# Kernel tuning notes

Measured on AMD Instinct MI355X. Metric: run time of the kernel, lower is better.

Reference implementation:

```python
import jax, jax.numpy as jnp
import numpy as np

B, N, D, T, M, V, K, HB, FF, L, H = 64, 32, 512, 8, 20, 512, 8, 16, 2048, 2, 8
SCALE = 1.0 / np.sqrt(D // H)


def _ln(x, g, b, eps=1e-5):
    m = x.mean(-1, keepdims=True)
    v = ((x - m) ** 2).mean(-1, keepdims=True)
    return (x - m) / jnp.sqrt(v + eps) * g + b


def _heads(x):
    return x.reshape(x.shape[:-1] + (H, D // H))


def setup_inputs():
    ks = iter(jax.random.split(jax.random.key(0), 60))
    def rn(shape, s=1.0):
        return jax.random.normal(next(ks), shape, jnp.float32) * s
    d = {}
    d['ego_query'] = rn((B, 1, D))
    d['agents_query'] = rn((B, N, D))
    d['bev_feature'] = rn((B, D, HB, HB))
    d['agent_states'] = rn((B, N, 8)) * 10.0
    d['agent_labels'] = rn((B, N))
    d['gt_traj'] = rn((B, T, 3))
    d['codebook'] = rn((V, 2), 0.1)
    for p in ['ego_ctx', 'bevproj', 'agent']:
        d[p + '_w'] = rn((D, D), 0.02); d[p + '_b'] = jnp.zeros((D,))
        d[p + '_g'] = jnp.ones((D,)); d[p + '_beta'] = jnp.zeros((D,))
    d['tok_emb'] = rn((V, D), 0.02)
    d['step_e'] = rn((T, D), 0.02)
    d['mode_e'] = rn((M, D), 0.02)
    d['role_e'] = rn((2, D), 0.02)
    d['bos_e'] = rn((1, D), 0.02)
    for p in ['t', 'e', 'v']:
        d[p + '_qkv_w'] = rn((L, 3 * D, D), 0.02); d[p + '_qkv_b'] = jnp.zeros((L, 3 * D))
        d[p + '_out_w'] = rn((L, D, D), 0.02); d[p + '_out_b'] = jnp.zeros((L, D))
        d[p + '_g'] = jnp.ones((L, D)); d[p + '_beta'] = jnp.zeros((L, D))
    d['ffn_w1'] = rn((L, FF, D), 0.02); d['ffn_b1'] = jnp.zeros((L, FF))
    d['ffn_w2'] = rn((L, D, FF), 0.02); d['ffn_b2'] = jnp.zeros((L, D))
    d['ffn_g'] = jnp.ones((L, D)); d['ffn_beta'] = jnp.zeros((L, D))
    d['head_w'] = rn((V, D), 0.02); d['head_b'] = jnp.zeros((V,))
    return d


def reference(ego_query, agents_query, bev_feature, agent_states, agent_labels, gt_traj, codebook,
              ego_ctx_w, ego_ctx_b, ego_ctx_g, ego_ctx_beta,
              bevproj_w, bevproj_b, bevproj_g, bevproj_beta,
              agent_w, agent_b, agent_g, agent_beta,
              tok_emb, step_e, mode_e, role_e, bos_e,
              t_qkv_w, t_qkv_b, t_out_w, t_out_b, t_g, t_beta,
              e_qkv_w, e_qkv_b, e_out_w, e_out_b, e_g, e_beta,
              v_qkv_w, v_qkv_b, v_out_w, v_out_b, v_g, v_beta,
              ffn_w1, ffn_b1, ffn_w2, ffn_b2, ffn_g, ffn_beta,
              head_w, head_b):
    Bd = ego_query.shape[0]
    P = HB * HB
    # BEV tokens [B, P, D]
    bev = jnp.transpose(bev_feature.reshape(Bd, D, P), (0, 2, 1))
    bev = jax.nn.relu(_ln(bev @ bevproj_w.T + bevproj_b, bevproj_g, bevproj_beta))
    # top-K nearest valid agents
    valid = jax.nn.sigmoid(agent_labels) > 0.05
    dist = jnp.where(valid, jnp.linalg.norm(agent_states[..., :2], axis=-1), jnp.inf)
    _, idx = jax.lax.top_k(-dist, K)
    topk_valid = jnp.take_along_axis(valid, idx, axis=1)
    agent_ctx = jnp.take_along_axis(agents_query, idx[..., None], axis=1)  # [B,K,D]
    agent_enc = jax.nn.relu(_ln(agent_ctx @ agent_w.T + agent_b, agent_g, agent_beta))
    agent_kv = agent_enc[:, :, None, :] + step_e[None, None] + role_e[1][None, None, None]  # [B,K,T,D]
    ego_base = jax.nn.relu(_ln(ego_query[:, 0] @ ego_ctx_w.T + ego_ctx_b, ego_ctx_g, ego_ctx_beta))
    # sequential codebook matching (accumulated-position NN scan, no grad)
    gt_pos = jnp.broadcast_to(gt_traj[:, None, :, :2], (Bd, M, T, 2))
    cb = jax.lax.stop_gradient(codebook)
    def cb_step(acc, pos_t):
        dsq = ((acc[:, :, None, :] + cb[None, None] - pos_t[:, :, None, :]) ** 2).sum(-1)  # [B,M,V]
        ii = jnp.argmin(dsq, axis=-1)
        return acc + cb[ii], ii
    _, idxs = jax.lax.scan(cb_step, jnp.zeros((Bd, M, 2), gt_pos.dtype),
                           jnp.moveaxis(jax.lax.stop_gradient(gt_pos), 2, 0))
    tokens = jnp.transpose(idxs, (1, 2, 0))  # [B,M,T]
    # teacher-forced input embeddings
    bos = bos_e[0][None, :] + ego_base  # [B,D]
    inp = jnp.concatenate([jnp.broadcast_to(bos[:, None, None, :], (Bd, M, 1, D)),
                           tok_emb[tokens[:, :, :-1]]], axis=2)
    ego_q = inp + step_e[None, None] + role_e[0][None, None, None] + mode_e[None, :, None, :]
    caus = jnp.triu(jnp.full((T, T), -jnp.inf, ego_q.dtype), 1)
    inv = ~topk_valid
    inv = inv & ~inv.all(axis=-1, keepdims=True)  # guard: never mask everything
    for i in range(L):
        # temporal causal self-attention over T
        qw, kw, vw = jnp.split(t_qkv_w[i], 3, 0); qb, kb, vb = jnp.split(t_qkv_b[i], 3, 0)
        Q, Kh, Vh = _heads(ego_q @ qw.T + qb), _heads(ego_q @ kw.T + kb), _heads(ego_q @ vw.T + vb)
        s = jnp.einsum('bmqhe,bmkhe->bmhqk', Q, Kh) * SCALE + caus
        o = jnp.einsum('bmhqk,bmkhe->bmqhe', jax.nn.softmax(s, -1), Vh).reshape(ego_q.shape)
        ego_q = _ln(ego_q + o @ t_out_w[i].T + t_out_b[i], t_g[i], t_beta[i])
        # ego-to-agent cross-attention (kv varies per step t)
        qw, kw, vw = jnp.split(e_qkv_w[i], 3, 0); qb, kb, vb = jnp.split(e_qkv_b[i], 3, 0)
        Q = _heads(ego_q @ qw.T + qb)  # [B,M,T,H,e]
        Kh, Vh = _heads(agent_kv @ kw.T + kb), _heads(agent_kv @ vw.T + vb)  # [B,K,T,H,e]
        s = jnp.einsum('bmthe,bkthe->bmhtk', Q, Kh) * SCALE
        s = jnp.where(inv[:, None, None, None, :], -jnp.inf, s)
        o = jnp.einsum('bmhtk,bkthe->bmthe', jax.nn.softmax(s, -1), Vh).reshape(ego_q.shape)
        ego_q = _ln(ego_q + o @ e_out_w[i].T + e_out_b[i], e_g[i], e_beta[i])
        # BEV cross-attention
        qw, kw, vw = jnp.split(v_qkv_w[i], 3, 0); qb, kb, vb = jnp.split(v_qkv_b[i], 3, 0)
        Q = _heads(ego_q @ qw.T + qb)
        Kh, Vh = _heads(bev @ kw.T + kb), _heads(bev @ vw.T + vb)  # [B,P,H,e]
        s = jnp.einsum('bmthe,bphe->bmhtp', Q, Kh) * SCALE
        o = jnp.einsum('bmhtp,bphe->bmthe', jax.nn.softmax(s, -1), Vh).reshape(ego_q.shape)
        ego_q = _ln(ego_q + o @ v_out_w[i].T + v_out_b[i], v_g[i], v_beta[i])
        # FFN
        hid = jax.nn.gelu(ego_q @ ffn_w1[i].T + ffn_b1[i], approximate=False)
        ego_q = _ln(ego_q + hid @ ffn_w2[i].T + ffn_b2[i], ffn_g[i], ffn_beta[i])
    return ego_q @ head_w.T + head_b  # token logits [B,M,T,V]
```

## Files before the change

kernel.cpp:

```cpp
#include <hip/hip_runtime.h>
#include <hip/hip_bf16.h>
#include <math.h>
#include <type_traits>

typedef __hip_bfloat16 bf16;
typedef __attribute__((ext_vector_type(8))) short bf16x8;
typedef __attribute__((ext_vector_type(4))) float f32x4;

__device__ __forceinline__ float b2f(bf16 x){ return __bfloat162float(x); }
__device__ __forceinline__ short f2s(float f){
  bf16 h = __float2bfloat16(f);
  short s; __builtin_memcpy(&s, &h, 2); return s;
}
__device__ __forceinline__ float u2f(unsigned short u){ union { unsigned int i; float f; } z; z.i = ((unsigned int)u) << 16; return z.f; }
__device__ __forceinline__ bf16x8 cvt8(float4 a, float4 b){
  return (bf16x8){f2s(a.x),f2s(a.y),f2s(a.z),f2s(a.w), f2s(b.x),f2s(b.y),f2s(b.z),f2s(b.w)};
}

struct WSrc { const float* p[12]; };
__global__ __launch_bounds__(256) void k_cvtw(WSrc srcs, bf16* __restrict__ dst){
  const unsigned off[13] = {0u,262144u,524288u,786432u,2359296u,2883584u,4456448u,4980736u,
                            6553600u,7077888u,9175040u,11272192u,11534336u};
  size_t base = ((size_t)blockIdx.x*256 + threadIdx.x)*8;
  int seg = 0;
  while (seg < 11 && base >= off[seg+1]) seg++;
  const float* s = srcs.p[seg] + (base - off[seg]);
  float4 a = *(const float4*)s;
  float4 b = *(const float4*)(s + 4);
  *(bf16x8*)&dst[base] = cvt8(a, b);
}

template<typename AT, typename WT, typename CT, int ACT, int BN, int RES>
__global__ __launch_bounds__(256, BN == 64 ? 2 : 1)
void k_gemm_mfma(const AT* __restrict__ A, const WT* __restrict__ W,
                 const float* __restrict__ bias, CT* C,
                 const float* Rres, int rows, int Kd, int Nc)
{
  __shared__ short As[128][40];
  __shared__ short Bs[BN][40];
  constexpr int NI = BN / 32;
  int rb = blockIdx.x * 128, nb = blockIdx.y * BN;
  int tid = threadIdx.x;
  int l = tid & 63, w = tid >> 6;
  int wr = (w >> 1) * 64, wc = (w & 1) * (BN/2);
  int lr = l & 15, lk = l >> 4;
  f32x4 acc[4][NI];
  #pragma unroll
  for (int i = 0; i < 4; i++)
    #pragma unroll
    for (int j = 0; j < NI; j++)
      acc[i][j] = (f32x4){0.f, 0.f, 0.f, 0.f};
  int sr = tid >> 1;
  int sc = (tid & 1) * 16;
  bool doB = (BN == 128) || (tid < 128);
  bool doA = (rb + sr) < rows;

  float4 faA[4], fbA[4], faB[4], fbB[4];
  bf16x8 baA[2], baB[2], wbA[2], wbB[2];
  #pragma unroll
  for (int i = 0; i < 4; i++){ faA[i] = (float4){0,0,0,0}; fbA[i] = (float4){0,0,0,0};
                               faB[i] = (float4){0,0,0,0}; fbB[i] = (float4){0,0,0,0}; }
  baA[0] = baA[1] = baB[0] = baB[1] = (bf16x8){0,0,0,0,0,0,0,0};
  wbA[0] = wbA[1] = wbB[0] = wbB[1] = (bf16x8){0,0,0,0,0,0,0,0};

  auto LOADS = [&](float4* fa, bf16x8* ba, float4* fb, bf16x8* wb, int k0){
    if constexpr (std::is_same<AT, float>::value){
      if (doA){
        const float4* p = (const float4*)(A + (size_t)(rb + sr)*Kd + k0 + sc);
        fa[0] = p[0]; fa[1] = p[1]; fa[2] = p[2]; fa[3] = p[3];
      }
    } else {
      if (doA){
        const bf16x8* p = (const bf16x8*)((const unsigned short*)A + (size_t)(rb + sr)*Kd + k0 + sc);
        ba[0] = p[0]; ba[1] = p[1];
      }
    }
    if (doB){
      if constexpr (std::is_same<WT, float>::value){
        const float4* p = (const float4*)(W + (size_t)(nb + sr)*Kd + k0 + sc);
        fb[0] = p[0]; fb[1] = p[1]; fb[2] = p[2]; fb[3] = p[3];
      } else {
        const bf16x8* p = (const bf16x8*)((const unsigned short*)W + (size_t)(nb + sr)*Kd + k0 + sc);
        wb[0] = p[0]; wb[1] = p[1];
      }
    }
  };
  auto STOREK = [&](float4* fa, bf16x8* ba, float4* fb, bf16x8* wb){
    if constexpr (std::is_same<AT, float>::value){
      *(bf16x8*)&As[sr][sc]     = cvt8(fa[0], fa[1]);
      *(bf16x8*)&As[sr][sc + 8] = cvt8(fa[2], fa[3]);
    } else {
      *(bf16x8*)&As[sr][sc]     = ba[0];
      *(bf16x8*)&As[sr][sc + 8] = ba[1];
    }
    if (doB){
      if constexpr (std::is_same<WT, float>::value){
        *(bf16x8*)&Bs[sr][sc]     = cvt8(fb[0], fb[1]);
        *(bf16x8*)&Bs[sr][sc + 8] = cvt8(fb[2], fb[3]);
      } else {
        *(bf16x8*)&Bs[sr][sc]     = wb[0];
        *(bf16x8*)&Bs[sr][sc + 8] = wb[1];
      }
    }
  };
  auto COMPUTE = [&](){
    bf16x8 af[4], bf_[NI];
    #pragma unroll
    for (int mi = 0; mi < 4; mi++) af[mi]  = *(const bf16x8*)&As[wr + mi*16 + lr][lk*8];
    #pragma unroll
    for (int ni = 0; ni < NI; ni++) bf_[ni] = *(const bf16x8*)&Bs[wc + ni*16 + lr][lk*8];
    #pragma unroll
    for (int mi = 0; mi < 4; mi++)
      #pragma unroll
      for (int ni = 0; ni < NI; ni++)
        acc[mi][ni] = __builtin_amdgcn_mfma_f32_16x16x32_bf16(af[mi], bf_[ni], acc[mi][ni], 0, 0, 0);
  };

  int nst = Kd >> 5;
  LOADS(faA, baA, fbA, wbA, 0);
  LOADS(faB, baB, fbB, wbB, 32);
  for (int s = 0; s < nst; s += 2){
    __syncthreads();
    STOREK(faA, baA, fbA, wbA);
    __syncthreads();
    if (s + 2 < nst) LOADS(faA, baA, fbA, wbA, (s+2)*32);
    COMPUTE();
    __syncthreads();
    STOREK(faB, baB, fbB, wbB);
    __syncthreads();
    if (s + 3 < nst) LOADS(faB, baB, fbB, wbB, (s+3)*32);
    COMPUTE();
  }

  #pragma unroll
  for (int mi = 0; mi < 4; mi++){
    #pragma unroll
    for (int ni = 0; ni < NI; ni++){
      int col = nb + wc + ni*16 + lr;
      float bs = bias[col];
      #pragma unroll
      for (int r = 0; r < 4; r++){
        int row = rb + wr + mi*16 + lk*4 + r;
        if (row < rows){
          float v = acc[mi][ni][r] + bs;
          if (RES) v += Rres[(size_t)row*Nc + col];
          if (ACT == 1) v = 0.5f*v*(1.0f + erff(v*0.70710678118654752f));
          if constexpr (std::is_same<CT, float>::value) C[(size_t)row*Nc + col] = v;
          else C[(size_t)row*Nc + col] = __float2bfloat16(v);
        }
      }
    }
  }
}

template<typename AT, typename WT, typename CT, int ACT, int RES>
__global__ __launch_bounds__(256, 4)
void k_gemm64(const AT* __restrict__ A, const WT* __restrict__ W,
              const float* __restrict__ bias, CT* C,
              const float* Rres, int rows, int Kd, int Nc)
{
  __shared__ short As[64][40];
  __shared__ short Bs[64][40];
  int rb = blockIdx.x * 64, nb = blockIdx.y * 64;
  int tid = threadIdx.x;
  int l = tid & 63, w = tid >> 6;
  int wr = (w >> 1) * 32, wc = (w & 1) * 32;
  int lr = l & 15, lk = l >> 4;
  f32x4 acc[2][2];
  #pragma unroll
  for (int i = 0; i < 2; i++)
    #pragma unroll
    for (int j = 0; j < 2; j++)
      acc[i][j] = (f32x4){0.f, 0.f, 0.f, 0.f};
  int sr = tid >> 2;
  int sc = (tid & 3) * 8;
  bool doA = (rb + sr) < rows;

  float4 faA[2], faB[2], fwA[2], fwB[2];
  bf16x8 baA, baB, wbA, wbB;
  faA[0]=faA[1]=faB[0]=faB[1]=(float4){0,0,0,0};
  fwA[0]=fwA[1]=fwB[0]=fwB[1]=(float4){0,0,0,0};
  baA = baB = wbA = wbB = (bf16x8){0,0,0,0,0,0,0,0};

  auto LOADS = [&](float4* fa, bf16x8& ba, float4* fw, bf16x8& wb, int k0){
    if constexpr (std::is_same<AT, float>::value){
      if (doA){
        const float4* p = (const float4*)(A + (size_t)(rb + sr)*Kd + k0 + sc);
        fa[0] = p[0]; fa[1] = p[1];
      }
    } else {
      if (doA) ba = *(const bf16x8*)((const unsigned short*)A + (size_t)(rb + sr)*Kd + k0 + sc);
    }
    if constexpr (std::is_same<WT, float>::value){
      const float4* p = (const float4*)(W + (size_t)(nb + sr)*Kd + k0 + sc);
      fw[0] = p[0]; fw[1] = p[1];
    } else {
      wb = *(const bf16x8*)((const unsigned short*)W + (size_t)(nb + sr)*Kd + k0 + sc);
    }
  };
  auto STOREK = [&](float4* fa, bf16x8& ba, float4* fw, bf16x8& wb){
    if constexpr (std::is_same<AT, float>::value) *(bf16x8*)&As[sr][sc] = cvt8(fa[0], fa[1]);
    else                                          *(bf16x8*)&As[sr][sc] = ba;
    if constexpr (std::is_same<WT, float>::value) *(bf16x8*)&Bs[sr][sc] = cvt8(fw[0], fw[1]);
    else                                          *(bf16x8*)&Bs[sr][sc] = wb;
  };
  auto COMPUTE = [&](){
    bf16x8 af[2], bf_[2];
    #pragma unroll
    for (int mi = 0; mi < 2; mi++) af[mi]  = *(const bf16x8*)&As[wr + mi*16 + lr][lk*8];
    #pragma unroll
    for (int ni = 0; ni < 2; ni++) bf_[ni] = *(const bf16x8*)&Bs[wc + ni*16 + lr][lk*8];
    #pragma unroll
    for (int mi = 0; mi < 2; mi++)
      #pragma unroll
      for (int ni = 0; ni < 2; ni++)
        acc[mi][ni] = __builtin_amdgcn_mfma_f32_16x16x32_bf16(af[mi], bf_[ni], acc[mi][ni], 0, 0, 0);
  };

  int nst = Kd >> 5;
  LOADS(faA, baA, fwA, wbA, 0);
  LOADS(faB, baB, fwB, wbB, 32);
  for (int s = 0; s < nst; s += 2){
    __syncthreads();
    STOREK(faA, baA, fwA, wbA);
    __syncthreads();
    if (s + 2 < nst) LOADS(faA, baA, fwA, wbA, (s+2)*32);
    COMPUTE();
    __syncthreads();
    STOREK(faB, baB, fwB, wbB);
    __syncthreads();
    if (s + 3 < nst) LOADS(faB, baB, fwB, wbB, (s+3)*32);
    COMPUTE();
  }

  #pragma unroll
  for (int mi = 0; mi < 2; mi++){
    #pragma unroll
    for (int ni = 0; ni < 2; ni++){
      int col = nb + wc + ni*16 + lr;
      float bs = bias[col];
      #pragma unroll
      for (int r = 0; r < 4; r++){
        int row = rb + wr + mi*16 + lk*4 + r;
        if (row < rows){
          float v = acc[mi][ni][r] + bs;
          if (RES) v += Rres[(size_t)row*Nc + col];
          if (ACT == 1) v = 0.5f*v*(1.0f + erff(v*0.70710678118654752f));
          if constexpr (std::is_same<CT, float>::value) C[(size_t)row*Nc + col] = v;
          else C[(size_t)row*Nc + col] = __float2bfloat16(v);
        }
      }
    }
  }
}

template<typename XT, typename OT>
__global__ __launch_bounds__(256) void k_ln(const XT* X, const float* R,
                                            const float* g, const float* bt,
                                            OT* out, int relu)
{
  __shared__ float red[4];
  int row = blockIdx.x, t = threadIdx.x;
  size_t base = (size_t)row * 512;
  float x0, x1;
  if constexpr (std::is_same<XT, float>::value){ x0 = X[base + t]; x1 = X[base + t + 256]; }
  else { x0 = b2f(X[base + t]); x1 = b2f(X[base + t + 256]); }
  if (R){ x0 += R[base + t]; x1 += R[base + t + 256]; }
  float v = x0 + x1;
  #pragma unroll
  for (int o = 32; o > 0; o >>= 1) v += __shfl_xor(v, o);
  if ((t & 63) == 0) red[t >> 6] = v;
  __syncthreads();
  float mean = (red[0]+red[1]+red[2]+red[3]) * (1.0f/512.0f);
  float d0 = x0 - mean, d1 = x1 - mean;
  v = d0*d0 + d1*d1;
  #pragma unroll
  for (int o = 32; o > 0; o >>= 1) v += __shfl_xor(v, o);
  __syncthreads();
  if ((t & 63) == 0) red[t >> 6] = v;
  __syncthreads();
  float var = (red[0]+red[1]+red[2]+red[3]) * (1.0f/512.0f);
  float is = 1.0f / sqrtf(var + 1e-5f);
  float y0 = d0*is*g[t] + bt[t];
  float y1 = d1*is*g[t+256] + bt[t+256];
  if (relu){ y0 = fmaxf(y0, 0.0f); y1 = fmaxf(y1, 0.0f); }
  if constexpr (std::is_same<OT, float>::value){ out[base + t] = y0; out[base + t + 256] = y1; }
  else { out[base + t] = __float2bfloat16(y0); out[base + t + 256] = __float2bfloat16(y1); }
}

__global__ void k_bev_tok(const float* __restrict__ bev, bf16* __restrict__ out){
  __shared__ float tile[32][33];
  int b = blockIdx.z;
  int d0 = blockIdx.x * 32;
  int p0 = blockIdx.y * 32;
  int tx = threadIdx.x, ty = threadIdx.y;
  #pragma unroll
  for (int i = 0; i < 4; i++){
    int d = d0 + ty + i*8;
    tile[ty + i*8][tx] = bev[((size_t)b*512 + d)*256 + p0 + tx];
  }
  __syncthreads();
  #pragma unroll
  for (int i = 0; i < 4; i++){
    int p = p0 + ty + i*8;
    out[((size_t)b*256 + p)*512 + d0 + tx] = __float2bfloat16(tile[tx][ty + i*8]);
  }
}

__global__ void k_topk(const float* __restrict__ labels, const float* __restrict__ states,
                       int* __restrict__ idxo, int* __restrict__ invo)
{
  __shared__ float dist[32];
  __shared__ int valid[32];
  int b = blockIdx.x, t = threadIdx.x;
  if (t < 32){
    float lab = labels[b*32 + t];
    float sg = 1.0f / (1.0f + expf(-lab));
    int va = sg > 0.05f;
    float x = states[((size_t)b*32 + t)*8 + 0];
    float y = states[((size_t)b*32 + t)*8 + 1];
    float d = sqrtf(__fadd_rn(__fmul_rn(x,x), __fmul_rn(y,y)));
    dist[t] = va ? d : INFINITY;
    valid[t] = va;
  }
  __syncthreads();
  if (t == 0){
    unsigned used = 0;
    int inv8[8]; int allinv = 1;
    for (int kk = 0; kk < 8; kk++){
      float best = INFINITY; int bi = -1;
      for (int i = 0; i < 32; i++){
        if (used & (1u << i)) continue;
        if (bi < 0 || dist[i] < best){ best = dist[i]; bi = i; }
      }
      used |= 1u << bi;
      idxo[b*8 + kk] = bi;
      inv8[kk] = !valid[bi];
      allinv &= inv8[kk];
    }
    for (int kk = 0; kk < 8; kk++) invo[b*8 + kk] = allinv ? 0 : inv8[kk];
  }
}

__global__ void k_gather(const float* __restrict__ aq, const int* __restrict__ idx, bf16* __restrict__ out)
{
  int rk = blockIdx.x; int b = rk >> 3;
  int src = idx[rk] & 31;
  int t = threadIdx.x;
  size_t sbase = ((size_t)(b*32 + src))*512;
  out[(size_t)rk*512 + t]       = __float2bfloat16(aq[sbase + t]);
  out[(size_t)rk*512 + t + 256] = __float2bfloat16(aq[sbase + t + 256]);
}

__global__ void k_agentkv(const float* __restrict__ enc, const float* __restrict__ step_e,
                          const float* __restrict__ role_e, bf16* __restrict__ out)
{
  int row = blockIdx.x;
  int t8 = row & 7; int bk = row >> 3;
  int tx = threadIdx.x;
  #pragma unroll
  for (int j = 0; j < 2; j++){
    int d = tx + j*256;
    out[(size_t)row*512 + d] = __float2bfloat16((enc[(size_t)bk*512 + d] + step_e[t8*512 + d]) + role_e[512 + d]);
  }
}

__global__ __launch_bounds__(64) void k_cbscan(const float* __restrict__ gt, const float* __restrict__ cb,
                                               int* __restrict__ toks)
{
  __shared__ float cbx[512], cby[512];
  int b = blockIdx.x;
  int l = threadIdx.x;
  #pragma unroll
  for (int i = 0; i < 8; i++){
    int v = l + i*64;
    cbx[v] = cb[v*2 + 0];
    cby[v] = cb[v*2 + 1];
  }
  __syncthreads();
  float ax = 0.0f, ay = 0.0f;
  for (int t = 0; t < 8; t++){
    float px = gt[(b*8 + t)*3 + 0];
    float py = gt[(b*8 + t)*3 + 1];
    float bestv = INFINITY; int besti = 0;
    #pragma unroll
    for (int i = 0; i < 8; i++){
      int v = l*8 + i;
      float dx = __fsub_rn(__fadd_rn(ax, cbx[v]), px);
      float dy = __fsub_rn(__fadd_rn(ay, cby[v]), py);
      float d = __fadd_rn(__fmul_rn(dx,dx), __fmul_rn(dy,dy));
      if (d < bestv || (d == bestv && v < besti)){ bestv = d; besti = v; }
    }
    #pragma unroll
    for (int o = 32; o > 0; o >>= 1){
      float ov = __shfl_xor(bestv, o);
      int oi = __shfl_xor(besti, o);
      if (ov < bestv || (ov == bestv && oi < besti)){ bestv = ov; besti = oi; }
    }
    ax = __fadd_rn(ax, cbx[besti]);
    ay = __fadd_rn(ay, cby[besti]);
    if (l == 0) toks[b*8 + t] = besti;
  }
}

__global__ void k_embed(const int* __restrict__ toks, const float* __restrict__ ebase,
                        const float* __restrict__ tok_emb, const float* __restrict__ step_e,
                        const float* __restrict__ mode_e, const float* __restrict__ role_e,
                        const float* __restrict__ bos_e, float* __restrict__ out)
{
  int row = blockIdx.x;
  int t = row & 7; int bm = row >> 3; int m = bm % 20; int b = bm / 20;
  int tok = (t == 0) ? 0 : (toks[b*8 + t - 1] & 511);
  int tx = threadIdx.x;
  #pragma unroll
  for (int j = 0; j < 2; j++){
    int d = tx + j*256;
    float base = (t == 0) ? (bos_e[d] + ebase[(size_t)b*512 + d])
                          : tok_emb[(size_t)tok*512 + d];
    out[(size_t)row*512 + d] = ((base + step_e[t*512 + d]) + role_e[d]) + mode_e[m*512 + d];
  }
}

__global__ __launch_bounds__(64) void k_tattn(const bf16* __restrict__ QKV, bf16* __restrict__ O)
{
  __shared__ float q[8][65], k[8][65], v[8][65], w[8][9];
  int h = blockIdx.x & 7; int bm = blockIdx.x >> 3;
  int l = threadIdx.x;
  for (int t = 0; t < 8; t++){
    size_t base = ((size_t)(bm*8 + t))*1536 + h*64 + l;
    q[t][l] = b2f(QKV[base]);
    k[t][l] = b2f(QKV[base + 512]);
    v[t][l] = b2f(QKV[base + 1024]);
  }
  __syncthreads();
  int tq = l >> 3, tk = l & 7;
  float s = -INFINITY;
  if (tk <= tq){
    float acc = 0.0f;
    #pragma unroll
    for (int e = 0; e < 64; e++) acc += q[tq][e]*k[tk][e];
    s = acc * 0.125f;
  }
  float mx = s;
  #pragma unroll
  for (int o = 1; o < 8; o <<= 1) mx = fmaxf(mx, __shfl_xor(mx, o));
  float ex = (tk <= tq) ? expf(s - mx) : 0.0f;
  float sm = ex;
  #pragma unroll
  for (int o = 1; o < 8; o <<= 1) sm += __shfl_xor(sm, o);
  w[tq][tk] = ex / sm;
  __syncthreads();
  #pragma unroll
  for (int t2 = 0; t2 < 8; t2++){
    float acc = 0.0f;
    #pragma unroll
    for (int tk2 = 0; tk2 < 8; tk2++) acc += w[t2][tk2]*v[tk2][l];
    O[((size_t)(bm*8 + t2))*512 + h*64 + l] = __float2bfloat16(acc);
  }
}

__global__ __launch_bounds__(64) void k_eattn(const bf16* __restrict__ Q, const bf16* __restrict__ KV,
                                              const int* __restrict__ inv,
                                              bf16* __restrict__ O, int row0)
{
  int blk = blockIdx.x;
  int h = blockIdx.y;
  int grow = row0 + blk;
  int t = grow & 7;
  int b = grow / 160;
  int l = threadIdx.x;
  size_t qoff = (size_t)blk*512 + h*64 + l;
  float q = b2f(Q[qoff]);
  float s[8];
  #pragma unroll
  for (int k = 0; k < 8; k++){
    float p = q * b2f(KV[((size_t)((b*8 + k)*8 + t))*1024 + h*64 + l]);
    #pragma unroll
    for (int o = 32; o > 0; o >>= 1) p += __shfl_xor(p, o);
    s[k] = p * 0.125f;
  }
  float mx = -INFINITY;
  #pragma unroll
  for (int k = 0; k < 8; k++){
    if (inv[b*8 + k]) s[k] = -INFINITY;
    mx = fmaxf(mx, s[k]);
  }
  float sum = 0.0f, w[8];
  #pragma unroll
  for (int k = 0; k < 8; k++){ w[k] = expf(s[k] - mx); sum += w[k]; }
  float rs = 1.0f / sum;
  float acc = 0.0f;
  #pragma unroll
  for (int k = 0; k < 8; k++)
    acc += (w[k]*rs) * b2f(KV[((size_t)((b*8 + k)*8 + t))*1024 + 512 + h*64 + l]);
  O[qoff] = __float2bfloat16(acc);
}

__global__ __launch_bounds__(256, 2) void k_vattn(const bf16* __restrict__ Q, const bf16* __restrict__ KV,
                                                  bf16* __restrict__ O)
{
  __shared__ unsigned short Ks[256][72];
  __shared__ unsigned short Vt[64][264];
  __shared__ float red[2][2][16];
  unsigned short (*P_lds)[264] = (unsigned short (*)[264])&Ks[0][0];

  int bl = blockIdx.x, h = blockIdx.y, qz = blockIdx.z;
  int tid = threadIdx.x;
  const unsigned short* KVr = (const unsigned short*)KV;

  {
    const uint4* ksrc = (const uint4*)&KVr[((size_t)(bl*256 + tid))*1024 + h*64];
    const uint4* vsrc = (const uint4*)&KVr[((size_t)(bl*256 + tid))*1024 + 512 + h*64];
    #pragma unroll
    for (int i = 0; i < 8; i++){
      uint4 kx = ksrc[i];
      *(uint4*)&Ks[tid][i*8] = kx;
    }
    #pragma unroll
    for (int i = 0; i < 8; i++){
      uint4 vx = vsrc[i];
      unsigned short vs[8];
      __builtin_memcpy(vs, &vx, 16);
      #pragma unroll
      for (int j = 0; j < 8; j++) Vt[i*8 + j][tid] = vs[j];
    }
  }
  __syncthreads();

  int w = tid >> 6, l = tid & 63, lr = l & 15, lk = l >> 4;
  int mt = w >> 1, ch = w & 1;

  int qrow = bl*160 + qz*32 + mt*16 + lr;
  const unsigned short* Qr = (const unsigned short*)Q;
  bf16x8 qf0 = *(const bf16x8*)&Qr[(size_t)qrow*512 + h*64 + lk*8];
  bf16x8 qf1 = *(const bf16x8*)&Qr[(size_t)qrow*512 + h*64 + 32 + lk*8];

  f32x4 sacc[8];
  #pragma unroll
  for (int nt = 0; nt < 8; nt++) sacc[nt] = (f32x4){0.f,0.f,0.f,0.f};
  #pragma unroll
  for (int nt = 0; nt < 8; nt++){
    int key0 = ch*128 + nt*16 + lr;
    bf16x8 kf0 = *(const bf16x8*)&Ks[key0][lk*8];
    bf16x8 kf1 = *(const bf16x8*)&Ks[key0][32 + lk*8];
    sacc[nt] = __builtin_amdgcn_mfma_f32_16x16x32_bf16(qf0, kf0, sacc[nt], 0, 0, 0);
    sacc[nt] = __builtin_amdgcn_mfma_f32_16x16x32_bf16(qf1, kf1, sacc[nt], 0, 0, 0);
  }

  float rmax[4] = {-INFINITY, -INFINITY, -INFINITY, -INFINITY};
  #pragma unroll
  for (int nt = 0; nt < 8; nt++)
    #pragma unroll
    for (int r = 0; r < 4; r++){
      float v = sacc[nt][r] * 0.125f;
      sacc[nt][r] = v;
      rmax[r] = fmaxf(rmax[r], v);
    }
  #pragma unroll
  for (int r = 0; r < 4; r++){
    #pragma unroll
    for (int o = 1; o < 16; o <<= 1) rmax[r] = fmaxf(rmax[r], __shfl_xor(rmax[r], o));
  }
  if (lr == 0){
    #pragma unroll
    for (int r = 0; r < 4; r++) red[mt][ch][lk*4 + r] = rmax[r];
  }
  __syncthreads();
  float m4[4];
  #pragma unroll
  for (int r = 0; r < 4; r++) m4[r] = fmaxf(red[mt][0][lk*4 + r], red[mt][1][lk*4 + r]);
  float rsum[4] = {0.f, 0.f, 0.f, 0.f};
  #pragma unroll
  for (int nt = 0; nt < 8; nt++){
    #pragma unroll
    for (int r = 0; r < 4; r++){
      float e = expf(sacc[nt][r] - m4[r]);
      rsum[r] += e;
      P_lds[mt*16 + lk*4 + r][ch*128 + nt*16 + lr] = (unsigned short)f2s(e);
    }
  }
  #pragma unroll
  for (int r = 0; r < 4; r++){
    #pragma unroll
    for (int o = 1; o < 16; o <<= 1) rsum[r] += __shfl_xor(rsum[r], o);
  }
  __syncthreads();
  if (lr == 0){
    #pragma unroll
    for (int r = 0; r < 4; r++) red[mt][ch][lk*4 + r] = rsum[r];
  }
  __syncthreads();
  float rcp4[4];
  #pragma unroll
  for (int r = 0; r < 4; r++) rcp4[r] = 1.0f / (red[mt][0][lk*4 + r] + red[mt][1][lk*4 + r]);

  f32x4 oacc0 = (f32x4){0.f,0.f,0.f,0.f};
  f32x4 oacc1 = (f32x4){0.f,0.f,0.f,0.f};
  #pragma unroll
  for (int kk = 0; kk < 8; kk++){
    bf16x8 pf  = *(const bf16x8*)&P_lds[mt*16 + lr][kk*32 + lk*8];
    bf16x8 vf0 = *(const bf16x8*)&Vt[ch*32 + lr][kk*32 + lk*8];
    bf16x8 vf1 = *(const bf16x8*)&Vt[ch*32 + 16 + lr][kk*32 + lk*8];
    oacc0 = __builtin_amdgcn_mfma_f32_16x16x32_bf16(pf, vf0, oacc0, 0, 0, 0);
    oacc1 = __builtin_amdgcn_mfma_f32_16x16x32_bf16(pf, vf1, oacc1, 0, 0, 0);
  }

  {
    size_t obase = ((size_t)(bl*160 + qz*32 + mt*16 + lk*4))*512 + h*64 + ch*32 + lr;
    #pragma unroll
    for (int r = 0; r < 4; r++){
      O[obase + (size_t)r*512]      = __float2bfloat16(oacc0[r] * rcp4[r]);
      O[obase + (size_t)r*512 + 16] = __float2bfloat16(oacc1[r] * rcp4[r]);
    }
  }
}

template<typename AT, typename CT, int ACT, int BN, int RES>
static inline void launch_gemm(bool wbf, const AT* A, const float* Wf, const bf16* Wb,
                               const float* bias, CT* C, const float* Rr,
                               int rows, int Kd, int Nc, hipStream_t st){
  dim3 g((rows + 127)/128, Nc/BN);
  if (wbf) k_gemm_mfma<AT,bf16,CT,ACT,BN,RES><<<g,256,0,st>>>(A, Wb, bias, C, Rr, rows, Kd, Nc);
  else     k_gemm_mfma<AT,float,CT,ACT,BN,RES><<<g,256,0,st>>>(A, Wf, bias, C, Rr, rows, Kd, Nc);
}
template<typename AT, typename CT, int ACT, int RES>
static inline void launch_gemm64(bool wbf, const AT* A, const float* Wf, const bf16* Wb,
                                 const float* bias, CT* C, const float* Rr,
                                 int rows, int Kd, int Nc, hipStream_t st){
  dim3 g((rows + 63)/64, Nc/64);
  if (wbf) k_gemm64<AT,bf16,CT,ACT,RES><<<g,256,0,st>>>(A, Wb, bias, C, Rr, rows, Kd, Nc);
  else     k_gemm64<AT,float,CT,ACT,RES><<<g,256,0,st>>>(A, Wf, bias, C, Rr, rows, Kd, Nc);
}

extern "C" void kernel_launch(void* const* d_in, const int* in_sizes, int n_in,
                              void* d_out, int out_size, void* d_ws, size_t ws_size,
                              hipStream_t stream)
{
  (void)in_sizes; (void)n_in; (void)out_size;
  const float* ego_query    = (const float*)d_in[0];
  const float* agents_query = (const float*)d_in[1];
  const float* bev_feature  = (const float*)d_in[2];
  const float* agent_states = (const float*)d_in[3];
  const float* agent_labels = (const float*)d_in[4];
  const float* gt_traj      = (const float*)d_in[5];
  const float* codebook     = (const float*)d_in[6];
  const float* ego_ctx_w    = (const float*)d_in[7];
  const float* ego_ctx_b    = (const float*)d_in[8];
  const float* ego_ctx_g    = (const float*)d_in[9];
  const float* ego_ctx_beta = (const float*)d_in[10];
  const float* bevproj_w    = (const float*)d_in[11];
  const float* bevproj_b    = (const float*)d_in[12];
  const float* bevproj_g    = (const float*)d_in[13];
  const float* bevproj_beta = (const float*)d_in[14];
  const float* agent_w      = (const float*)d_in[15];
  const float* agent_b      = (const float*)d_in[16];
  const float* agent_g      = (const float*)d_in[17];
  const float* agent_beta   = (const float*)d_in[18];
  const float* tok_emb      = (const float*)d_in[19];
  const float* step_e       = (const float*)d_in[20];
  const float* mode_e       = (const float*)d_in[21];
  const float* role_e       = (const float*)d_in[22];
  const float* bos_e        = (const float*)d_in[23];
  const float* t_qkv_w      = (const float*)d_in[24];
  const float* t_qkv_b      = (const float*)d_in[25];
  const float* t_out_w      = (const float*)d_in[26];
  const float* t_out_b      = (const float*)d_in[27];
  const float* t_g          = (const float*)d_in[28];
  const float* t_beta       = (const float*)d_in[29];
  const float* e_qkv_w      = (const float*)d_in[30];
  const float* e_qkv_b      = (const float*)d_in[31];
  const float* e_out_w      = (const float*)d_in[32];
  const float* e_out_b      = (const float*)d_in[33];
  const float* e_g          = (const float*)d_in[34];
  const float* e_beta       = (const float*)d_in[35];
  const float* v_qkv_w      = (const float*)d_in[36];
  const float* v_qkv_b      = (const float*)d_in[37];
  const float* v_out_w      = (const float*)d_in[38];
  const float* v_out_b      = (const float*)d_in[39];
  const float* v_g          = (const float*)d_in[40];
  const float* v_beta       = (const float*)d_in[41];
  const float* ffn_w1       = (const float*)d_in[42];
  const float* ffn_b1       = (const float*)d_in[43];
  const float* ffn_w2       = (const float*)d_in[44];
  const float* ffn_b2       = (const float*)d_in[45];
  const float* ffn_g        = (const float*)d_in[46];
  const float* ffn_beta     = (const float*)d_in[47];
  const float* head_w       = (const float*)d_in[48];
  const float* head_b       = (const float*)d_in[49];

  const size_t NEEDED       = 46274560;
  const size_t NEEDED_BIG   = 67248128;
  const size_t NEEDED_BIG2  = 100800512;
  const size_t NEEDED_BIG3  = 123869184;
  if (ws_size < NEEDED) return;
  bool big  = ws_size >= NEEDED_BIG;
  bool big2 = ws_size >= NEEDED_BIG2;
  bool big3 = ws_size >= NEEDED_BIG3;
  int RC  = big ? 10240 : 5120;
  int NCH = big ? 1 : 2;

  char* WB = (char*)d_ws;
  bf16*  bevtok = (bf16*)(WB + 0);
  bf16*  akv    = (bf16*)(WB + 16777216);
  float* ebase  = (float*)(WB + 20971520);
  char*  ARENA  = WB + 21102592;
  bf16*  KVb    = (bf16*)(WB + 37879808);
  bf16*  KVbig  = (bf16*)(WB + 67239936);
  bf16*  WCV    = (bf16*)(WB + 100800512);
  size_t tk0    = big2 ? 100794368 : (big ? 67239936 : 46268416);
  int*   toks   = (int*)(WB + tk0);
  int*   idxb   = (int*)(WB + tk0 + 2048);
  int*   invb   = (int*)(WB + tk0 + 4096);
  size_t oe_off = big ? 31457280 : 5242880;

  float* egoq = (float*)d_out;

  bf16* c_bevproj = WCV + 0;
  bf16* c_ego     = WCV + 262144;
  bf16* c_agent   = WCV + 524288;
  bf16* c_tqkv    = WCV + 786432;
  bf16* c_tout    = WCV + 2359296;
  bf16* c_eqkv    = WCV + 2883584;
  bf16* c_eout    = WCV + 4456448;
  bf16* c_vqkv    = WCV + 4980736;
  bf16* c_vout    = WCV + 6553600;
  bf16* c_ffn1    = WCV + 7077888;
  bf16* c_ffn2    = WCV + 9175040;
  bf16* c_head    = WCV + 11272192;

  if (big3){
    WSrc src;
    src.p[0] = bevproj_w; src.p[1] = ego_ctx_w; src.p[2] = agent_w;  src.p[3] = t_qkv_w;
    src.p[4] = t_out_w;   src.p[5] = e_qkv_w;   src.p[6] = e_out_w;  src.p[7] = v_qkv_w;
    src.p[8] = v_out_w;   src.p[9] = ffn_w1;    src.p[10] = ffn_w2;  src.p[11] = head_w;
    k_cvtw<<<5632, 256, 0, stream>>>(src, WCV);
  }

  #define GEMM(AT,CT,ACT,BN,RES, Ap, Wf, Wb, Bp,Cp,Rp, R,K,N) \
    launch_gemm<AT,CT,ACT,BN,RES>(big3, Ap, Wf, Wb, Bp, Cp, Rp, R, K, N, stream)
  #define GEMM64(AT,CT,ACT,RES, Ap, Wf, Wb, Bp,Cp,Rp, R,K,N) \
    launch_gemm64<AT,CT,ACT,RES>(big3, Ap, Wf, Wb, Bp, Cp, Rp, R, K, N, stream)

  {
    bf16* raw = (bf16*)ARENA;
    k_bev_tok<<<dim3(16, 8, 64), dim3(32, 8), 0, stream>>>(bev_feature, raw);
    GEMM64(bf16,bf16,0,0, raw, bevproj_w, c_bevproj, bevproj_b, bevtok, nullptr, 16384, 512, 512);
    k_ln<bf16,bf16><<<16384, 256, 0, stream>>>(bevtok, nullptr, bevproj_g, bevproj_beta, bevtok, 1);
  }

  GEMM64(float,float,0,0, ego_query, ego_ctx_w, c_ego, ego_ctx_b, (float*)ARENA, nullptr, 64, 512, 512);
  k_ln<float,float><<<64, 256, 0, stream>>>((float*)ARENA, nullptr, ego_ctx_g, ego_ctx_beta, ebase, 1);

  k_topk<<<64, 64, 0, stream>>>(agent_labels, agent_states, idxb, invb);
  {
    bf16*  gat = (bf16*)ARENA;
    float* enc = (float*)(ARENA + 524288);
    k_gather<<<512, 256, 0, stream>>>(agents_query, idxb, gat);
    GEMM64(bf16,float,0,0, gat, agent_w, c_agent, agent_b, enc, nullptr, 512, 512, 512);
    k_ln<float,float><<<512, 256, 0, stream>>>(enc, nullptr, agent_g, agent_beta, enc, 1);
    k_agentkv<<<4096, 256, 0, stream>>>(enc, step_e, role_e, akv);
  }

  k_cbscan<<<64, 64, 0, stream>>>(gt_traj, codebook, toks);
  k_embed<<<10240, 256, 0, stream>>>(toks, ebase, tok_emb, step_e, mode_e, role_e, bos_e, egoq);

  for (int i = 0; i < 2; i++){
    {
      bf16* QKV = (bf16*)ARENA;
      bf16* Ot  = big ? (bf16*)(ARENA + oe_off) : KVb;
      for (int c = 0; c < NCH; c++){
        float* eg = egoq + (size_t)c*RC*512;
        GEMM(float,bf16,0,128,0, eg, t_qkv_w + (size_t)i*786432, c_tqkv + (size_t)i*786432,
             t_qkv_b + i*1536, QKV, nullptr, RC, 512, 1536);
        k_tattn<<<RC, 64, 0, stream>>>(QKV, Ot);
        GEMM64(bf16,float,0,1, Ot, t_out_w + (size_t)i*262144, c_tout + (size_t)i*262144,
             t_out_b + i*512, eg, eg, RC, 512, 512);
      }
      k_ln<float,float><<<10240, 256, 0, stream>>>(egoq, nullptr, t_g + i*512, t_beta + i*512, egoq, 0);
    }
    {
      const float* eqw = e_qkv_w + (size_t)i*786432;
      bf16*        eqc = c_eqkv + (size_t)i*786432;
      const float* eqb = e_qkv_b + i*1536;
      bf16* Qe = (bf16*)ARENA;
      bf16* Oe = (bf16*)(ARENA + oe_off);
      GEMM64(bf16,bf16,0,0, akv, eqw + 262144, eqc + 262144, eqb + 512, KVb, nullptr, 4096, 512, 1024);
      for (int c = 0; c < NCH; c++){
        float* eg = egoq + (size_t)c*RC*512;
        GEMM64(float,bf16,0,0, eg, eqw, eqc, eqb, Qe, nullptr, RC, 512, 512);
        k_eattn<<<dim3(RC, 8), 64, 0, stream>>>(Qe, KVb, invb, Oe, c*RC);
        GEMM64(bf16,float,0,1, Oe, e_out_w + (size_t)i*262144, c_eout + (size_t)i*262144,
             e_out_b + i*512, eg, eg, RC, 512, 512);
      }
      k_ln<float,float><<<10240, 256, 0, stream>>>(egoq, nullptr, e_g + i*512, e_beta + i*512, egoq, 0);
    }
    {
      const float* vqw = v_qkv_w + (size_t)i*786432;
      bf16*        vqc = c_vqkv + (size_t)i*786432;
      const float* vqb = v_qkv_b + i*1536;
      if (big2){
        bf16* Qv = (bf16*)ARENA;
        bf16* Ov = (bf16*)(ARENA + 10485760);
        GEMM64(bf16,bf16,0,0, bevtok, vqw + 262144, vqc + 262144, vqb + 512, KVbig, nullptr, 16384, 512, 1024);
        GEMM64(float,bf16,0,0, egoq, vqw, vqc, vqb, Qv, nullptr, 10240, 512, 512);
        k_vattn<<<dim3(64, 8, 5), 256, 0, stream>>>(Qv, KVbig, Ov);
        GEMM64(bf16,float,0,1, Ov, v_out_w + (size_t)i*262144, c_vout + (size_t)i*262144,
             v_out_b + i*512, egoq, egoq, 10240, 512, 512);
      } else {
        bf16* Qv = (bf16*)ARENA;
        bf16* Ov = (bf16*)(ARENA + 2621440);
        for (int gidx = 0; gidx < 4; gidx++){
          float* eg = egoq + (size_t)gidx*2560*512;
          GEMM64(bf16,bf16,0,0, bevtok + (size_t)gidx*4096*512, vqw + 262144, vqc + 262144,
               vqb + 512, KVb, nullptr, 4096, 512, 1024);
          GEMM64(float,bf16,0,0, eg, vqw, vqc, vqb, Qv, nullptr, 2560, 512, 512);
          k_vattn<<<dim3(16, 8, 5), 256, 0, stream>>>(Qv, KVb, Ov);
          GEMM64(bf16,float,0,1, Ov, v_out_w + (size_t)i*262144, c_vout + (size_t)i*262144,
               v_out_b + i*512, eg, eg, 2560, 512, 512);
        }
      }
      k_ln<float,float><<<10240, 256, 0, stream>>>(egoq, nullptr, v_g + i*512, v_beta + i*512, egoq, 0);
    }
    {
      bf16* hid = (bf16*)ARENA;
      for (int c = 0; c < NCH; c++){
        float* eg = egoq + (size_t)c*RC*512;
        GEMM(float,bf16,1,128,0, eg, ffn_w1 + (size_t)i*1048576, c_ffn1 + (size_t)i*1048576,
             ffn_b1 + i*2048, hid, nullptr, RC, 512, 2048);
        GEMM64(bf16,float,0,1, hid, ffn_w2 + (size_t)i*1048576, c_ffn2 + (size_t)i*1048576,
             ffn_b2 + i*512, eg, eg, RC, 2048, 512);
      }
      if (i == 0){
        k_ln<float,float><<<10240, 256, 0, stream>>>(egoq, nullptr, ffn_g, ffn_beta, egoq, 0);
      } else {
        k_ln<float,bf16><<<10240, 256, 0, stream>>>(egoq, nullptr, ffn_g + 512, ffn_beta + 512, (bf16*)ARENA, 0);
      }
    }
  }

  GEMM64(bf16,float,0,0, (bf16*)ARENA, head_w, c_head, head_b, (float*)d_out, nullptr, 10240, 512, 512);
  #undef GEMM
  #undef GEMM64
}
```

Baseline: 1.017 ms.

## Double-buffer LDS tiles in MFMA GEMMs to halve barriers per K-step

Switches both GEMM kernels from a single shared tile with two register prefetch sets to ping-pong LDS buffers with one register prefetch set. Each K-step now needs one __syncthreads instead of two, and the store to the next LDS buffer can overlap compute on the current one. The cost is doubled LDS footprint, which may lower occupancy, especially for the 128-row kernel, while register use drops.

New measurement: 1.001 ms. About the same (-1.6%).

```diff
diff --git a/kernel.cpp b/kernel.cpp
--- a/kernel.cpp
+++ b/kernel.cpp
@@ -36,8 +36,8 @@
                  const float* __restrict__ bias, CT* C,
                  const float* Rres, int rows, int Kd, int Nc)
 {
-  __shared__ short As[128][40];
-  __shared__ short Bs[BN][40];
+  __shared__ short As[2][128][40];
+  __shared__ short Bs[2][BN][40];
   constexpr int NI = BN / 32;
   int rb = blockIdx.x * 128, nb = blockIdx.y * BN;
   int tid = threadIdx.x;
@@ -55,15 +55,13 @@
   bool doB = (BN == 128) || (tid < 128);
   bool doA = (rb + sr) < rows;
 
-  float4 faA[4], fbA[4], faB[4], fbB[4];
-  bf16x8 baA[2], baB[2], wbA[2], wbB[2];
-  #pragma unroll
-  for (int i = 0; i < 4; i++){ faA[i] = (float4){0,0,0,0}; fbA[i] = (float4){0,0,0,0};
-                               faB[i] = (float4){0,0,0,0}; fbB[i] = (float4){0,0,0,0}; }
-  baA[0] = baA[1] = baB[0] = baB[1] = (bf16x8){0,0,0,0,0,0,0,0};
-  wbA[0] = wbA[1] = wbB[0] = wbB[1] = (bf16x8){0,0,0,0,0,0,0,0};
-
-  auto LOADS = [&](float4* fa, bf16x8* ba, float4* fb, bf16x8* wb, int k0){
+  float4 fa[4], fb[4];
+  bf16x8 ba[2], wb[2];
+  #pragma unroll
+  for (int i = 0; i < 4; i++){ fa[i] = (float4){0,0,0,0}; fb[i] = (float4){0,0,0,0}; }
+  ba[0] = ba[1] = wb[0] = wb[1] = (bf16x8){0,0,0,0,0,0,0,0};
+
+  auto LOADS = [&](int k0){
     if constexpr (std::is_same<AT, float>::value){
       if (doA){
         const float4* p = (const float4*)(A + (size_t)(rb + sr)*Kd + k0 + sc);
@@ -85,30 +83,30 @@
       }
     }
   };
-  auto STOREK = [&](float4* fa, bf16x8* ba, float4* fb, bf16x8* wb){
+  auto STOREK = [&](int buf){
     if constexpr (std::is_same<AT, float>::value){
-      *(bf16x8*)&As[sr][sc]     = cvt8(fa[0], fa[1]);
-      *(bf16x8*)&As[sr][sc + 8] = cvt8(fa[2], fa[3]);
+      *(bf16x8*)&As[buf][sr][sc]     = cvt8(fa[0], fa[1]);
+      *(bf16x8*)&As[buf][sr][sc + 8] = cvt8(fa[2], fa[3]);
     } else {
-      *(bf16x8*)&As[sr][sc]     = ba[0];
-      *(bf16x8*)&As[sr][sc + 8] = ba[1];
+      *(bf16x8*)&As[buf][sr][sc]     = ba[0];
+      *(bf16x8*)&As[buf][sr][sc + 8] = ba[1];
     }
     if (doB){
       if constexpr (std::is_same<WT, float>::value){
-        *(bf16x8*)&Bs[sr][sc]     = cvt8(fb[0], fb[1]);
-        *(bf16x8*)&Bs[sr][sc + 8] = cvt8(fb[2], fb[3]);
+        *(bf16x8*)&Bs[buf][sr][sc]     = cvt8(fb[0], fb[1]);
+        *(bf16x8*)&Bs[buf][sr][sc + 8] = cvt8(fb[2], fb[3]);
       } else {
-        *(bf16x8*)&Bs[sr][sc]     = wb[0];
-        *(bf16x8*)&Bs[sr][sc + 8] = wb[1];
+        *(bf16x8*)&Bs[buf][sr][sc]     = wb[0];
+        *(bf16x8*)&Bs[buf][sr][sc + 8] = wb[1];
       }
     }
   };
-  auto COMPUTE = [&](){
+  auto COMPUTE = [&](int buf){
     bf16x8 af[4], bf_[NI];
     #pragma unroll
-    for (int mi = 0; mi < 4; mi++) af[mi]  = *(const bf16x8*)&As[wr + mi*16 + lr][lk*8];
-    #pragma unroll
-    for (int ni = 0; ni < NI; ni++) bf_[ni] = *(const bf16x8*)&Bs[wc + ni*16 + lr][lk*8];
+    for (int mi = 0; mi < 4; mi++) af[mi]  = *(const bf16x8*)&As[buf][wr + mi*16 + lr][lk*8];
+    #pragma unroll
+    for (int ni = 0; ni < NI; ni++) bf_[ni] = *(const bf16x8*)&Bs[buf][wc + ni*16 + lr][lk*8];
     #pragma unroll
     for (int mi = 0; mi < 4; mi++)
       #pragma unroll
@@ -117,19 +115,17 @@
   };
 
   int nst = Kd >> 5;
-  LOADS(faA, baA, fbA, wbA, 0);
-  LOADS(faB, baB, fbB, wbB, 32);
-  for (int s = 0; s < nst; s += 2){
-    __syncthreads();
-    STOREK(faA, baA, fbA, wbA);
-    __syncthreads();
-    if (s + 2 < nst) LOADS(faA, baA, fbA, wbA, (s+2)*32);
-    COMPUTE();
-    __syncthreads();
-    STOREK(faB, baB, fbB, wbB);
-    __syncthreads();
-    if (s + 3 < nst) LOADS(faB, baB, fbB, wbB, (s+3)*32);
-    COMPUTE();
+  LOADS(0);
+  STOREK(0);
+  if (nst > 1) LOADS(32);
+  __syncthreads();
+  for (int s = 0; s < nst; s++){
+    COMPUTE(s & 1);
+    if (s + 1 < nst){
+      STOREK((s + 1) & 1);
+      if (s + 2 < nst) LOADS((s + 2) * 32);
+      __syncthreads();
+    }
   }
 
   #pragma unroll
@@ -159,8 +155,8 @@
               const float* __restrict__ bias, CT* C,
               const float* Rres, int rows, int Kd, int Nc)
 {
-  __shared__ short As[64][40];
-  __shared__ short Bs[64][40];
+  __shared__ short As[2][64][40];
+  __shared__ short Bs[2][64][40];
   int rb = blockIdx.x * 64, nb = blockIdx.y * 64;
   int tid = threadIdx.x;
   int l = tid & 63, w = tid >> 6;
@@ -176,13 +172,12 @@
   int sc = (tid & 3) * 8;
   bool doA = (rb + sr) < rows;
 
-  float4 faA[2], faB[2], fwA[2], fwB[2];
-  bf16x8 baA, baB, wbA, wbB;
-  faA[0]=faA[1]=faB[0]=faB[1]=(float4){0,0,0,0};
-  fwA[0]=fwA[1]=fwB[0]=fwB[1]=(float4){0,0,0,0};
-  baA = baB = wbA = wbB = (bf16x8){0,0,0,0,0,0,0,0};
-
-  auto LOADS = [&](float4* fa, bf16x8& ba, float4* fw, bf16x8& wb, int k0){
+  float4 fa[2], fw[2];
+  bf16x8 ba, wb;
+  fa[0] = fa[1] = fw[0] = fw[1] = (float4){0,0,0,0};
+  ba = wb = (bf16x8){0,0,0,0,0,0,0,0};
+
+  auto LOADS = [&](int k0){
     if constexpr (std::is_same<AT, float>::value){
       if (doA){
         const float4* p = (const float4*)(A + (size_t)(rb + sr)*Kd + k0 + sc);
@@ -198,18 +193,18 @@
       wb = *(const bf16x8*)((const unsigned short*)W + (size_t)(nb + sr)*Kd + k0 + sc);
     }
   };
-  auto STOREK = [&](float4* fa, bf16x8& ba, float4* fw, bf16x8& wb){
-    if constexpr (std::is_same<AT, float>::value) *(bf16x8*)&As[sr][sc] = cvt8(fa[0], fa[1]);
-    else                                          *(bf16x8*)&As[sr][sc] = ba;
-    if constexpr (std::is_same<WT, float>::value) *(bf16x8*)&Bs[sr][sc] = cvt8(fw[0], fw[1]);
-    else                                          *(bf16x8*)&Bs[sr][sc] = wb;
+  auto STOREK = [&](int buf){
+    if constexpr (std::is_same<AT, float>::value) *(bf16x8*)&As[buf][sr][sc] = cvt8(fa[0], fa[1]);
+    else                                          *(bf16x8*)&As[buf][sr][sc] = ba;
+    if constexpr (std::is_same<WT, float>::value) *(bf16x8*)&Bs[buf][sr][sc] = cvt8(fw[0], fw[1]);
+    else                                          *(bf16x8*)&Bs[buf][sr][sc] = wb;
   };
-  auto COMPUTE = [&](){
+  auto COMPUTE = [&](int buf){
     bf16x8 af[2], bf_[2];
     #pragma unroll
-    for (int mi = 0; mi < 2; mi++) af[mi]  = *(const bf16x8*)&As[wr + mi*16 + lr][lk*8];
-    #pragma unroll
-    for (int ni = 0; ni < 2; ni++) bf_[ni] = *(const bf16x8*)&Bs[wc + ni*16 + lr][lk*8];
+    for (int mi = 0; mi < 2; mi++) af[mi]  = *(const bf16x8*)&As[buf][wr + mi*16 + lr][lk*8];
+    #pragma unroll
+    for (int ni = 0; ni < 2; ni++) bf_[ni] = *(const bf16x8*)&Bs[buf][wc + ni*16 + lr][lk*8];
     #pragma unroll
     for (int mi = 0; mi < 2; mi++)
       #pragma unroll
@@ -218,19 +213,17 @@
   };
 
   int nst = Kd >> 5;
-  LOADS(faA, baA, fwA, wbA, 0);
-  LOADS(faB, baB, fwB, wbB, 32);
-  for (int s = 0; s < nst; s += 2){
-    __syncthreads();
-    STOREK(faA, baA, fwA, wbA);
-    __syncthreads();
-    if (s + 2 < nst) LOADS(faA, baA, fwA, wbA, (s+2)*32);
-    COMPUTE();
-    __syncthreads();
-    STOREK(faB, baB, fwB, wbB);
-    __syncthreads();
-    if (s + 3 < nst) LOADS(faB, baB, fwB, wbB, (s+3)*32);
-    COMPUTE();
+  LOADS(0);
+  STOREK(0);
+  if (nst > 1) LOADS(32);
+  __syncthreads();
+  for (int s = 0; s < nst; s++){
+    COMPUTE(s & 1);
+    if (s + 1 < nst){
+      STOREK((s + 1) & 1);
+      if (s + 2 < nst) LOADS((s + 2) * 32);
+      __syncthreads();
+    }
   }
 
   #pragma unroll
```
